# Optimization experiments

Measured on AMD Instinct MI355X. Metric: run time of the kernel, lower is better.

## Reference

```python
import jax, jax.numpy as jnp
import numpy as np

B, S, D, H = 4, 1024, 1024, 16
DK = D // H
NEG = -1e9


def setup_inputs() -> dict:
    key = jax.random.key(0)
    ks = jax.random.split(key, 8)
    inp = {
        "query": jax.random.normal(ks[0], (B, S, D), dtype=jnp.float32),
        "key": jax.random.normal(ks[1], (B, S, D), dtype=jnp.float32),
        "value": jax.random.normal(ks[2], (B, S, D), dtype=jnp.float32),
        "mask": jax.random.randint(ks[3], (B, S, S), 0, 2, dtype=jnp.int32),
        # bias-free Linear weights, torch layout [out, in]; y = x @ W.T
        "Wq": jax.random.normal(ks[4], (D, D), dtype=jnp.float32) / np.sqrt(D),
        "Wk": jax.random.normal(ks[5], (D, D), dtype=jnp.float32) / np.sqrt(D),
        "Wv": jax.random.normal(ks[6], (D, D), dtype=jnp.float32) / np.sqrt(D),
        "Wo": jax.random.normal(ks[7], (D, D), dtype=jnp.float32) / np.sqrt(D),
    }
    return inp


def _split_heads(x):
    # [B, S, D] -> [B, H, S, DK]
    return x.reshape(B, -1, H, DK).transpose(0, 2, 1, 3)


def reference(query, key, value, mask, Wq, Wk, Wv, Wo):
    q = _split_heads(query @ Wq.T)
    k = _split_heads(key @ Wk.T)
    v = _split_heads(value @ Wv.T)
    scores = jnp.einsum("bhqd,bhkd->bhqk", q, k) / jnp.sqrt(jnp.float32(DK))
    scores = jnp.where(mask[:, None, :, :] == 0, NEG, scores)
    p_attn = jax.nn.softmax(scores, axis=-1)
    x = jnp.einsum("bhqk,bhkd->bhqd", p_attn, v)
    x = x.transpose(0, 2, 1, 3).reshape(B, -1, D)
    # dropout p=0.0 (eval-equivalent): identity
    return x @ Wo.T
```

## Files before the change

kernel.cpp:

```cpp
#include <hip/hip_runtime.h>

#define BB 4
#define SS 1024
#define DD 1024
#define HH 16
#define DKK 64
#define MM (BB*SS)

typedef __bf16 bf16;
typedef __bf16 bf16x8 __attribute__((ext_vector_type(8)));
typedef float f32x4 __attribute__((ext_vector_type(4)));
typedef float f32x16 __attribute__((ext_vector_type(16)));

__device__ __forceinline__ f32x4 mfma16(bf16x8 a, bf16x8 b, f32x4 c) {
  return __builtin_amdgcn_mfma_f32_16x16x32_bf16(a, b, c, 0, 0, 0);
}
__device__ __forceinline__ f32x16 mfma32(bf16x8 a, bf16x8 b, f32x16 c) {
  return __builtin_amdgcn_mfma_f32_32x32x16_bf16(a, b, c, 0, 0, 0);
}
__device__ __forceinline__ float fexp2(float x) {
  return __builtin_amdgcn_exp2f(x);
}
__device__ __forceinline__ void gld_lds16(const bf16* g, bf16* l) {
  __builtin_amdgcn_global_load_lds(
      (const __attribute__((address_space(1))) void*)g,
      (__attribute__((address_space(3))) void*)l, 16, 0, 0);
}

__global__ __launch_bounds__(256)
void k_prep(const float* __restrict__ s0, const float* __restrict__ s1,
            const float* __restrict__ s2, const float* __restrict__ s3,
            const float* __restrict__ s4, const float* __restrict__ s5,
            const float* __restrict__ s6,
            bf16* __restrict__ d0, bf16* __restrict__ d1, bf16* __restrict__ d2,
            bf16* __restrict__ d3, bf16* __restrict__ d4, bf16* __restrict__ d5,
            bf16* __restrict__ d6,
            const int* __restrict__ mask, unsigned* __restrict__ bits) {
  const int t = blockIdx.y;
  if (t < 7) {
    const float* s = (t == 0) ? s0 : (t == 1) ? s1 : (t == 2) ? s2
                   : (t == 3) ? s3 : (t == 4) ? s4 : (t == 5) ? s5 : s6;
    bf16* d = (t == 0) ? d0 : (t == 1) ? d1 : (t == 2) ? d2
            : (t == 3) ? d3 : (t == 4) ? d4 : (t == 5) ? d5 : d6;
    const int n = (t < 3) ? (MM * DD) : (DD * DD);
    const int i0 = (blockIdx.x * 256 + threadIdx.x) * 8;
    if (i0 >= n) return;
    const f32x4 a = *(const f32x4*)(s + i0);
    const f32x4 bvv = *(const f32x4*)(s + i0 + 4);
    bf16x8 o;
#pragma unroll
    for (int j = 0; j < 4; ++j) { o[j] = (bf16)a[j]; o[4 + j] = (bf16)bvv[j]; }
    *(bf16x8*)(d + i0) = o;
    return;
  }
  const int tid = threadIdx.x;
  const int lane = tid & 63, wv = tid >> 6;
#pragma unroll
  for (int rr = 0; rr < 2; ++rr) {
    const int row = blockIdx.x * 2 + rr;
    const int b = row >> 10, q = row & 1023;
    const int qblk = q >> 6, qt = (q >> 5) & 1, l = q & 31;
    const size_t base = ((size_t)(b * 16 + qblk) * 2 + qt) * 4;
#pragma unroll
    for (int it = 0; it < 4; ++it) {
      const int cb = it * 256 + wv * 64;
      unsigned long long bal = __ballot(mask[(size_t)row * SS + cb + lane] != 0);
      if (lane == 0) {
        const int c0 = cb >> 5;
#pragma unroll
        for (int dd = 0; dd < 2; ++dd) {
          const int c = c0 + dd;
          bits[((base + (c >> 3)) * 8 + (c & 7)) * 32 + l] =
              (unsigned)(bal >> (32 * dd));
        }
      }
    }
  }
}

__global__ __launch_bounds__(256) void k_mask_bits(const int* __restrict__ mask,
                                                   unsigned* __restrict__ bits) {
  const int row = blockIdx.x;
  const int b = row >> 10, q = row & 1023;
  const int qblk = q >> 6, qt = (q >> 5) & 1, l = q & 31;
  const size_t base = ((size_t)(b * 16 + qblk) * 2 + qt) * 4;
  const int tid = threadIdx.x;
  const int lane = tid & 63, wv = tid >> 6;
#pragma unroll
  for (int it = 0; it < 4; ++it) {
    const int cb = it * 256 + wv * 64;
    unsigned long long bal = __ballot(mask[(size_t)row * SS + cb + lane] != 0);
    if (lane == 0) {
      const int c0 = cb >> 5;
#pragma unroll
      for (int dd = 0; dd < 2; ++dd) {
        const int c = c0 + dd;
        bits[((base + (c >> 3)) * 8 + (c & 7)) * 32 + l] =
            (unsigned)(bal >> (32 * dd));
      }
    }
  }
}

__global__ __launch_bounds__(256)
void k_kfrag(const bf16* __restrict__ K, bf16* __restrict__ Kf) {
  __shared__ bf16 Kl[32 * 66];
  const int kvb = blockIdx.x, h = blockIdx.y, b = blockIdx.z;
  const int tid = threadIdx.x;
  const int r = tid >> 3, c0 = (tid & 7) * 8;
  *(bf16x8*)&Kl[r * 66 + c0] =
      *(const bf16x8*)(K + (size_t)(b * SS + kvb * 32 + r) * DD + h * 64 + c0);
  __syncthreads();
  const int lane = tid & 63, l31 = lane & 31, hi = lane >> 5;
  const int kt = tid >> 6;
  bf16x8 ok;
#pragma unroll
  for (int j = 0; j < 8; ++j) ok[j] = Kl[l31 * 66 + kt * 16 + hi * 8 + j];
  *(bf16x8*)(Kf + ((size_t)((b * HH + h) * 32 + kvb)) * 2048 + tid * 8) = ok;
}

#define QSCALE 0.1803368801111204f

template<int AF32, int CF32>
__device__ __forceinline__ void gemm_body(const void* __restrict__ Ap,
                                          const float* __restrict__ Wp,
                                          void* __restrict__ Cp,
                                          int Mtot, int N, int K, int blk,
                                          float oscale) {
  __shared__ bf16 Al[128 * 40];
  __shared__ bf16 Bl[128 * 40];
  const int tid = threadIdx.x;
  const int lane = tid & 63;
  const int l15 = lane & 15, l4 = lane >> 4;
  const int wv = tid >> 6;
  const int nbm = Mtot >> 7;
  const int bm = blk % nbm, bn = blk / nbm;
  const size_t m0 = (size_t)bm << 7, n0 = (size_t)bn << 7;
  const int wr = (wv >> 1) << 6, wc = (wv & 1) << 6;
  const int srow = tid >> 2, scol = (tid & 3) << 3;

  f32x4 acc[4][4];
#pragma unroll
  for (int i = 0; i < 4; ++i)
#pragma unroll
    for (int j = 0; j < 4; ++j) acc[i][j] = f32x4{0.f, 0.f, 0.f, 0.f};

  for (int k0 = 0; k0 < K; k0 += 32) {
#pragma unroll
    for (int c = 0; c < 2; ++c) {
      const int row = (c << 6) + srow;
      bf16x8 av;
      if (AF32) {
        const float* s = (const float*)Ap + (m0 + row) * (size_t)K + k0 + scol;
        f32x4 v0 = *(const f32x4*)s;
        f32x4 v1 = *(const f32x4*)(s + 4);
#pragma unroll
        for (int j = 0; j < 4; ++j) { av[j] = (bf16)v0[j]; av[4 + j] = (bf16)v1[j]; }
      } else {
        av = *(const bf16x8*)((const bf16*)Ap + (m0 + row) * (size_t)K + k0 + scol);
      }
      *(bf16x8*)&Al[row * 40 + scol] = av;

      const float* ws_ = Wp + (n0 + row) * (size_t)K + k0 + scol;
      f32x4 w0 = *(const f32x4*)ws_;
      f32x4 w1 = *(const f32x4*)(ws_ + 4);
      bf16x8 wv8;
#pragma unroll
      for (int j = 0; j < 4; ++j) { wv8[j] = (bf16)w0[j]; wv8[4 + j] = (bf16)w1[j]; }
      *(bf16x8*)&Bl[row * 40 + scol] = wv8;
    }
    __syncthreads();

    bf16x8 af[4], bfv[4];
#pragma unroll
    for (int t = 0; t < 4; ++t) {
      af[t]  = *(const bf16x8*)&Al[(wr + t * 16 + l15) * 40 + l4 * 8];
      bfv[t] = *(const bf16x8*)&Bl[(wc + t * 16 + l15) * 40 + l4 * 8];
    }
    __builtin_amdgcn_s_setprio(1);
#pragma unroll
    for (int mt = 0; mt < 4; ++mt)
#pragma unroll
      for (int nt = 0; nt < 4; ++nt)
        acc[mt][nt] = mfma16(af[mt], bfv[nt], acc[mt][nt]);
    __builtin_amdgcn_s_setprio(0);
    __syncthreads();
  }

#pragma unroll
  for (int mt = 0; mt < 4; ++mt)
#pragma unroll
    for (int nt = 0; nt < 4; ++nt)
#pragma unroll
      for (int r = 0; r < 4; ++r) {
        const size_t row = m0 + wr + mt * 16 + l4 * 4 + r;
        const size_t col = n0 + wc + nt * 16 + l15;
        if (CF32) ((float*)Cp)[row * N + col] = acc[mt][nt][r];
        else      ((bf16*)Cp)[row * N + col] = (bf16)(acc[mt][nt][r] * oscale);
      }
}

__global__ __launch_bounds__(256)
void k_gemm_qkv(const float* __restrict__ A0, const float* __restrict__ A1,
                const float* __restrict__ A2, const float* __restrict__ W0,
                const float* __restrict__ W1, const float* __restrict__ W2,
                bf16* __restrict__ C0, bf16* __restrict__ C1, bf16* __restrict__ C2) {
  const int z = blockIdx.z;
  const float* A = (z == 0) ? A0 : (z == 1) ? A1 : A2;
  const float* W = (z == 0) ? W0 : (z == 1) ? W1 : W2;
  bf16* C = (z == 0) ? C0 : (z == 1) ? C1 : C2;
  const float sc = (z == 0) ? QSCALE : 1.0f;
  gemm_body<1, 0>(A, W, C, MM, DD, DD, blockIdx.x, sc);
}

__global__ __launch_bounds__(256)
void k_gemm_out(const bf16* __restrict__ A, const float* __restrict__ W,
                float* __restrict__ C) {
  gemm_body<0, 1>(A, W, C, MM, DD, DD, blockIdx.x, 1.0f);
}

__global__ __launch_bounds__(256)
void k_gemm_qkv_b16(const bf16* __restrict__ A0, const bf16* __restrict__ A1,
                    const bf16* __restrict__ A2, const bf16* __restrict__ W0,
                    const bf16* __restrict__ W1, const bf16* __restrict__ W2,
                    bf16* __restrict__ C0, bf16* __restrict__ Kf,
                    bf16* __restrict__ C2) {
  __shared__ bf16 Al[128 * 32];
  __shared__ bf16 Bl[128 * 32];
  const int z = blockIdx.z;
  const bf16* A = (z == 0) ? A0 : (z == 1) ? A1 : A2;
  const bf16* W = (z == 0) ? W0 : (z == 1) ? W1 : W2;
  const float oscale = (z == 0) ? QSCALE : 1.0f;

  const int tid = threadIdx.x, lane = tid & 63, w = tid >> 6;
  const int l15 = lane & 15, l4 = lane >> 4;
  const int bm = blockIdx.x & 31, bn = blockIdx.x >> 5;
  const size_t m0 = (size_t)bm << 7, n0 = (size_t)bn << 7;
  const int wr = (w >> 1) << 6, wc = (w & 1) << 6;
  const int srow = w * 32 + (lane >> 2);
  const int scol = (lane & 3) << 3;

  f32x4 acc[4][4];
#pragma unroll
  for (int i = 0; i < 4; ++i)
#pragma unroll
    for (int j = 0; j < 4; ++j) acc[i][j] = f32x4{0.f, 0.f, 0.f, 0.f};

  for (int k0 = 0; k0 < DD; k0 += 32) {
    const bf16* ga = A + (m0 + srow) * (size_t)DD + k0 + scol;
    const bf16* gb = W + (n0 + srow) * (size_t)DD + k0 + scol;
    gld_lds16(ga,            &Al[(w * 32) * 32]);
    gld_lds16(ga + 16 * DD,  &Al[(w * 32 + 16) * 32]);
    gld_lds16(gb,            &Bl[(w * 32) * 32]);
    gld_lds16(gb + 16 * DD,  &Bl[(w * 32 + 16) * 32]);
    __syncthreads();

    bf16x8 af[4], bfv[4];
#pragma unroll
    for (int t = 0; t < 4; ++t) {
      af[t]  = *(const bf16x8*)&Al[(wr + t * 16 + l15) * 32 + l4 * 8];
      bfv[t] = *(const bf16x8*)&Bl[(wc + t * 16 + l15) * 32 + l4 * 8];
    }
#pragma unroll
    for (int mt = 0; mt < 4; ++mt)
#pragma unroll
      for (int nt = 0; nt < 4; ++nt)
        acc[mt][nt] = mfma16(af[mt], bfv[nt], acc[mt][nt]);
    __syncthreads();
  }

  if (z != 1) {
    bf16* C = (z == 0) ? C0 : C2;
#pragma unroll
    for (int mt = 0; mt < 4; ++mt)
#pragma unroll
      for (int nt = 0; nt < 4; ++nt)
#pragma unroll
        for (int r = 0; r < 4; ++r) {
          const size_t row = m0 + wr + mt * 16 + l4 * 4 + r;
          const size_t col = n0 + wc + nt * 16 + l15;
          C[row * DD + col] = (bf16)(acc[mt][nt][r] * oscale);
        }
  } else {
#pragma unroll
    for (int mt = 0; mt < 4; ++mt)
#pragma unroll
      for (int nt = 0; nt < 4; ++nt)
#pragma unroll
        for (int r = 0; r < 4; ++r) {
          const int row = (int)m0 + wr + mt * 16 + l4 * 4 + r;
          const int col = (int)n0 + wc + nt * 16 + l15;
          const int b = row >> 10, kv = row & 1023;
          const int kvb = kv >> 5, l31 = kv & 31;
          const int h = col >> 6, dk = col & 63;
          const int kt = dk >> 4, hi = (dk >> 3) & 1, j = dk & 7;
          Kf[((size_t)((b * 16 + h) * 32 + kvb)) * 2048 + kt * 512 +
             (l31 + 32 * hi) * 8 + j] = (bf16)acc[mt][nt][r];
        }
  }
}

__global__ __launch_bounds__(256)
void k_gemm_out_b16(const bf16* __restrict__ A, const bf16* __restrict__ W,
                    float* __restrict__ C) {
  __shared__ bf16 Al[128 * 32];
  __shared__ bf16 Bl[128 * 32];
  const int tid = threadIdx.x, lane = tid & 63, w = tid >> 6;
  const int l15 = lane & 15, l4 = lane >> 4;
  const int bm = blockIdx.x & 31, bn = blockIdx.x >> 5;
  const size_t m0 = (size_t)bm << 7, n0 = (size_t)bn << 7;
  const int wr = (w >> 1) << 6, wc = (w & 1) << 6;
  const int srow = w * 32 + (lane >> 2);
  const int scol = (lane & 3) << 3;

  f32x4 acc[4][4];
#pragma unroll
  for (int i = 0; i < 4; ++i)
#pragma unroll
    for (int j = 0; j < 4; ++j) acc[i][j] = f32x4{0.f, 0.f, 0.f, 0.f};

  for (int k0 = 0; k0 < DD; k0 += 32) {
    const bf16* ga = A + (m0 + srow) * (size_t)DD + k0 + scol;
    const bf16* gb = W + (n0 + srow) * (size_t)DD + k0 + scol;
    gld_lds16(ga,            &Al[(w * 32) * 32]);
    gld_lds16(ga + 16 * DD,  &Al[(w * 32 + 16) * 32]);
    gld_lds16(gb,            &Bl[(w * 32) * 32]);
    gld_lds16(gb + 16 * DD,  &Bl[(w * 32 + 16) * 32]);
    __syncthreads();

    bf16x8 af[4], bfv[4];
#pragma unroll
    for (int t = 0; t < 4; ++t) {
      af[t]  = *(const bf16x8*)&Al[(wr + t * 16 + l15) * 32 + l4 * 8];
      bfv[t] = *(const bf16x8*)&Bl[(wc + t * 16 + l15) * 32 + l4 * 8];
    }
#pragma unroll
    for (int mt = 0; mt < 4; ++mt)
#pragma unroll
      for (int nt = 0; nt < 4; ++nt)
        acc[mt][nt] = mfma16(af[mt], bfv[nt], acc[mt][nt]);
    __syncthreads();
  }

#pragma unroll
  for (int mt = 0; mt < 4; ++mt)
#pragma unroll
    for (int nt = 0; nt < 4; ++nt)
#pragma unroll
      for (int r = 0; r < 4; ++r) {
        const size_t row = m0 + wr + mt * 16 + l4 * 4 + r;
        const size_t col = n0 + wc + nt * 16 + l15;
        C[row * DD + col] = acc[mt][nt][r];
      }
}

__global__ __launch_bounds__(256)
void k_attn(const bf16* __restrict__ Qw, const bf16* __restrict__ Kf,
            const bf16* __restrict__ Vw, const unsigned* __restrict__ mb,
            bf16* __restrict__ Xw) {
  __shared__ union {
    bf16 v[4][2048];
    struct { float o[64 * 33]; float l[4][64]; float inv[64]; } m;
  } sh;
  const int tid = threadIdx.x, lane = tid & 63, w = tid >> 6;
  const int l31 = lane & 31, hi = lane >> 5;
  const unsigned bid = blockIdx.x;
  const unsigned wg = (bid & 7) * 128 + (bid >> 3);
  const int bh = wg >> 4, qblk = wg & 15;
  const int h = bh & 15, b = bh >> 4;
  const int q0 = qblk * 64;

  bf16x8 qf[2][4];
#pragma unroll
  for (int qt = 0; qt < 2; ++qt) {
    const bf16* Qb = Qw + (size_t)(b * SS + q0 + qt * 32 + l31) * DD + h * 64 + hi * 8;
#pragma unroll
    for (int kt = 0; kt < 4; ++kt) qf[qt][kt] = *(const bf16x8*)(Qb + kt * 16);
  }
  const bf16* Kfb = Kf + ((size_t)((b * HH + h) * 32 + w * 8)) * 2048 + lane * 8;
  const bf16* Vg = Vw + (size_t)(b * SS) * DD + h * 64;
  const unsigned* mq0 = mb +
      ((size_t)(((b * 16 + qblk) * 2 + 0) * 4 + w) * 8) * 32 + l31;
  const unsigned* mq1 = mq0 + 1024;

  const int grow = lane >> 3;
  const int gcol = (lane & 7) * 8;
  const int kvw = w << 8;
  bf16* Vst = sh.v[w];

  f32x16 aco[2][2];
#pragma unroll
  for (int qt = 0; qt < 2; ++qt)
#pragma unroll
    for (int dt = 0; dt < 2; ++dt)
#pragma unroll
      for (int r = 0; r < 16; ++r) aco[qt][dt][r] = 0.f;
  float ssum[2] = { 0.f, 0.f };

  bf16x8 kf[4];
#pragma unroll
  for (int kt = 0; kt < 4; ++kt) kf[kt] = *(const bf16x8*)(Kfb + kt * 512);

  for (int t = 0; t < 8; ++t) {
    const int kv0 = kvw + t * 32;
#pragma unroll
    for (int i_ = 0; i_ < 4; ++i_)
      gld_lds16(Vg + (size_t)(kv0 + i_ * 8 + grow) * DD + gcol, Vst + i_ * 512);
    const unsigned mw0 = mq0[t * 32], mw1 = mq1[t * 32];

    bf16x8 va[2][2];
    union { bf16x8 v; int q[4]; } pa0[2], pa1[2];

#pragma unroll
    for (int qt = 0; qt < 2; ++qt) {
      f32x16 s;
#pragma unroll
      for (int r = 0; r < 16; ++r) s[r] = 0.f;
      __builtin_amdgcn_s_setprio(1);
#pragma unroll
      for (int kt = 0; kt < 4; ++kt) s = mfma32(kf[kt], qf[qt][kt], s);
      __builtin_amdgcn_s_setprio(0);

      if (qt == 1 && t < 7) {
        __builtin_amdgcn_sched_barrier(0);
        const bf16* tk = Kfb + (t + 1) * 2048;
#pragma unroll
        for (int kt = 0; kt < 4; ++kt) kf[kt] = *(const bf16x8*)(tk + kt * 512);
        __builtin_amdgcn_sched_barrier(0);
      }

      const unsigned mw = qt ? mw1 : mw0;
      float p[16];
#pragma unroll
      for (int r = 0; r < 16; ++r) {
        const int pos = (r & 3) + 8 * (r >> 2) + 4 * hi;
        p[r] = fexp2(((mw >> pos) & 1) ? s[r] : -1e9f);
      }
      {
        float a0 = (p[0] + p[1]) + (p[2] + p[3]);
        float a1 = (p[4] + p[5]) + (p[6] + p[7]);
        float a2 = (p[8] + p[9]) + (p[10] + p[11]);
        float a3 = (p[12] + p[13]) + (p[14] + p[15]);
        ssum[qt] += (a0 + a1) + (a2 + a3);
      }
      int dpk[8];
#pragma unroll
      for (int i = 0; i < 8; ++i) {
        union { bf16 hh[2]; int v; } u;
        u.hh[0] = (bf16)p[2 * i]; u.hh[1] = (bf16)p[2 * i + 1];
        dpk[i] = u.v;
      }
      const int sa = hi ? dpk[0] : dpk[2], sb = hi ? dpk[1] : dpk[3];
      const int sc_ = hi ? dpk[4] : dpk[6], sd = hi ? dpk[5] : dpk[7];
      const int ra = __shfl_xor(sa, 32), rb = __shfl_xor(sb, 32);
      const int rc = __shfl_xor(sc_, 32), rd = __shfl_xor(sd, 32);
      pa0[qt].q[0] = hi ? ra : dpk[0];  pa0[qt].q[1] = hi ? rb : dpk[1];
      pa0[qt].q[2] = hi ? dpk[2] : ra;  pa0[qt].q[3] = hi ? dpk[3] : rb;
      pa1[qt].q[0] = hi ? rc : dpk[4];  pa1[qt].q[1] = hi ? rd : dpk[5];
      pa1[qt].q[2] = hi ? dpk[6] : rc;  pa1[qt].q[3] = hi ? dpk[7] : rd;

      if (qt == 0) {
        asm volatile("s_waitcnt vmcnt(0)" ::: "memory");
        __builtin_amdgcn_sched_barrier(0);
#pragma unroll
        for (int dt = 0; dt < 2; ++dt)
#pragma unroll
          for (int s2 = 0; s2 < 2; ++s2) {
            bf16x8 tv;
#pragma unroll
            for (int j = 0; j < 8; ++j)
              tv[j] = Vst[(s2 * 16 + hi * 8 + j) * 64 + dt * 32 + l31];
            va[dt][s2] = tv;
          }
      }
      __builtin_amdgcn_s_setprio(1);
#pragma unroll
      for (int dt = 0; dt < 2; ++dt) {
        aco[qt][dt] = mfma32(va[dt][0], pa0[qt].v, aco[qt][dt]);
        aco[qt][dt] = mfma32(va[dt][1], pa1[qt].v, aco[qt][dt]);
      }
      __builtin_amdgcn_s_setprio(0);
    }
  }

#pragma unroll
  for (int qt = 0; qt < 2; ++qt) ssum[qt] += __shfl_xor(ssum[qt], 32);
  __syncthreads();
  if (hi == 0) {
#pragma unroll
    for (int qt = 0; qt < 2; ++qt) sh.m.l[w][qt * 32 + l31] = ssum[qt];
  }
  __syncthreads();
  if (w == 0) {
    sh.m.inv[lane] = 1.0f / (sh.m.l[0][lane] + sh.m.l[1][lane] +
                             sh.m.l[2][lane] + sh.m.l[3][lane]);
  }
  __syncthreads();
#pragma unroll
  for (int qt = 0; qt < 2; ++qt) {
    for (int rd2 = 0; rd2 < 4; ++rd2) {
      if (w == rd2) {
#pragma unroll
        for (int dt = 0; dt < 2; ++dt)
#pragma unroll
          for (int r = 0; r < 16; ++r) {
            const int d = dt * 32 + (r & 3) + 8 * (r >> 2) + 4 * hi;
            const int o = d * 33 + l31;
            if (rd2 == 0) sh.m.o[o] = aco[qt][dt][r];
            else          sh.m.o[o] += aco[qt][dt][r];
          }
      }
      __syncthreads();
    }
    {
      const int q = tid >> 3, d0 = (tid & 7) * 8;
      const float inv = sh.m.inv[qt * 32 + q];
      bf16x8 ov;
#pragma unroll
      for (int j = 0; j < 8; ++j) ov[j] = (bf16)(sh.m.o[(d0 + j) * 33 + q] * inv);
      *(bf16x8*)(Xw + (size_t)(b * SS + q0 + qt * 32 + q) * DD + h * 64 + d0) = ov;
    }
    __syncthreads();
  }
}

extern "C" void kernel_launch(void* const* d_in, const int* in_sizes, int n_in,
                              void* d_out, int out_size, void* d_ws, size_t ws_size,
                              hipStream_t stream) {
  const float* q32 = (const float*)d_in[0];
  const float* k32 = (const float*)d_in[1];
  const float* v32 = (const float*)d_in[2];
  const int* mask = (const int*)d_in[3];
  const float* Wq = (const float*)d_in[4];
  const float* Wk = (const float*)d_in[5];
  const float* Wv = (const float*)d_in[6];
  const float* Wo = (const float*)d_in[7];
  float* out = (float*)d_out;

  const size_t eAct = (size_t)MM * DD;
  const size_t eW = (size_t)DD * DD;

  bf16* Qb = (bf16*)d_ws;
  bf16* Kb = Qb + eAct;
  bf16* Vb = Kb + eAct;
  bf16* Xb = Vb + eAct;
  unsigned* mbits = (unsigned*)(Xb + eAct);
  bf16* Kfp = (bf16*)(mbits + (size_t)MM * 32);
  bf16* cvtBase = Kfp + eAct;
  bf16* Aq = cvtBase;
  bf16* Ak = Aq + eAct;
  bf16* Av = Ak + eAct;
  bf16* Wqb = Av + eAct;
  bf16* Wkb = Wqb + eW;
  bf16* Wvb = Wkb + eW;
  bf16* Wob = Wvb + eW;
  const size_t need = (size_t)((bf16*)(Wob + eW) - (bf16*)d_ws) * sizeof(bf16);

  if (ws_size >= need) {
    k_prep<<<dim3(2048, 8), 256, 0, stream>>>(q32, k32, v32, Wq, Wk, Wv, Wo,
                                              Aq, Ak, Av, Wqb, Wkb, Wvb, Wob,
                                              mask, mbits);
    k_gemm_qkv_b16<<<dim3(256, 1, 3), 256, 0, stream>>>(
        Aq, Ak, Av, Wqb, Wkb, Wvb, Qb, Kfp, Vb);
    k_attn<<<BB * HH * (SS / 64), 256, 0, stream>>>(Qb, Kfp, Vb, mbits, Xb);
    k_gemm_out_b16<<<256, 256, 0, stream>>>(Xb, Wob, out);
  } else {
    k_mask_bits<<<BB * SS, 256, 0, stream>>>(mask, mbits);
    k_gemm_qkv<<<dim3((MM / 128) * (DD / 128), 1, 3), 256, 0, stream>>>(
        q32, k32, v32, Wq, Wk, Wv, Qb, Kb, Vb);
    k_kfrag<<<dim3(32, HH, BB), 256, 0, stream>>>(Kb, Kfp);
    k_attn<<<BB * HH * (SS / 64), 256, 0, stream>>>(Qb, Kfp, Vb, mbits, Xb);
    k_gemm_out<<<(MM / 128) * (DD / 128), 256, 0, stream>>>(Xb, Wo, out);
  }
}
```

Measured before the change: 128.0 us.

## Pre-swizzle V into MFMA fragment layout and drop LDS staging in attention

The QKV GEMM epilogue now writes V directly in the per-lane MFMA fragment layout, matching how K was already stored, and the fallback path's fragment kernel handles both K and V. The attention kernel then loads V fragments with plain 16-byte global loads instead of staging V through LDS with a vmcnt wait and a per-element transposed read. K fragments are now loaded at the start of each iteration rather than prefetched one step ahead. This removes LDS traffic and a wait point, but loses the explicit K prefetch, uses more workspace, and makes the epilogue stores for V scattered.

```diff
diff --git a/kernel.cpp b/kernel.cpp
--- a/kernel.cpp
+++ b/kernel.cpp
@@ -103,20 +103,34 @@
 }
 
 __global__ __launch_bounds__(256)
-void k_kfrag(const bf16* __restrict__ K, bf16* __restrict__ Kf) {
+void k_frag(const bf16* __restrict__ K, const bf16* __restrict__ V,
+            bf16* __restrict__ Kf, bf16* __restrict__ Vf) {
   __shared__ bf16 Kl[32 * 66];
+  __shared__ bf16 Vl[32 * 66];
   const int kvb = blockIdx.x, h = blockIdx.y, b = blockIdx.z;
   const int tid = threadIdx.x;
   const int r = tid >> 3, c0 = (tid & 7) * 8;
-  *(bf16x8*)&Kl[r * 66 + c0] =
-      *(const bf16x8*)(K + (size_t)(b * SS + kvb * 32 + r) * DD + h * 64 + c0);
+  const size_t src = (size_t)(b * SS + kvb * 32 + r) * DD + h * 64 + c0;
+  *(bf16x8*)&Kl[r * 66 + c0] = *(const bf16x8*)(K + src);
+  *(bf16x8*)&Vl[r * 66 + c0] = *(const bf16x8*)(V + src);
   __syncthreads();
   const int lane = tid & 63, l31 = lane & 31, hi = lane >> 5;
-  const int kt = tid >> 6;
-  bf16x8 ok;
-#pragma unroll
-  for (int j = 0; j < 8; ++j) ok[j] = Kl[l31 * 66 + kt * 16 + hi * 8 + j];
-  *(bf16x8*)(Kf + ((size_t)((b * HH + h) * 32 + kvb)) * 2048 + tid * 8) = ok;
+  const size_t tb = ((size_t)((b * HH + h) * 32 + kvb)) * 2048 + tid * 8;
+  {
+    const int kt = tid >> 6;
+    bf16x8 ok;
+#pragma unroll
+    for (int j = 0; j < 8; ++j) ok[j] = Kl[l31 * 66 + kt * 16 + hi * 8 + j];
+    *(bf16x8*)(Kf + tb) = ok;
+  }
+  {
+    const int s2 = tid >> 7, dt = (tid >> 6) & 1;
+    bf16x8 ov;
+#pragma unroll
+    for (int j = 0; j < 8; ++j)
+      ov[j] = Vl[(s2 * 16 + hi * 8 + j) * 66 + dt * 32 + l31];
+    *(bf16x8*)(Vf + tb) = ov;
+  }
 }
 
 #define QSCALE 0.1803368801111204f
@@ -224,7 +238,7 @@
                     const bf16* __restrict__ A2, const bf16* __restrict__ W0,
                     const bf16* __restrict__ W1, const bf16* __restrict__ W2,
                     bf16* __restrict__ C0, bf16* __restrict__ Kf,
-                    bf16* __restrict__ C2) {
+                    bf16* __restrict__ Vf) {
   __shared__ bf16 Al[128 * 32];
   __shared__ bf16 Bl[128 * 32];
   const int z = blockIdx.z;
@@ -269,8 +283,7 @@
     __syncthreads();
   }
 
-  if (z != 1) {
-    bf16* C = (z == 0) ? C0 : C2;
+  if (z == 0) {
 #pragma unroll
     for (int mt = 0; mt < 4; ++mt)
 #pragma unroll
@@ -279,9 +292,9 @@
         for (int r = 0; r < 4; ++r) {
           const size_t row = m0 + wr + mt * 16 + l4 * 4 + r;
           const size_t col = n0 + wc + nt * 16 + l15;
-          C[row * DD + col] = (bf16)(acc[mt][nt][r] * oscale);
+          C0[row * DD + col] = (bf16)(acc[mt][nt][r] * oscale);
         }
-  } else {
+  } else if (z == 1) {
 #pragma unroll
     for (int mt = 0; mt < 4; ++mt)
 #pragma unroll
@@ -295,7 +308,24 @@
           const int h = col >> 6, dk = col & 63;
           const int kt = dk >> 4, hi = (dk >> 3) & 1, j = dk & 7;
           Kf[((size_t)((b * 16 + h) * 32 + kvb)) * 2048 + kt * 512 +
-             (l31 + 32 * hi) * 8 + j] = (bf16)acc[mt][nt][r];
+             (hi * 32 + l31) * 8 + j] = (bf16)acc[mt][nt][r];
+        }
+  } else {
+#pragma unroll
+    for (int mt = 0; mt < 4; ++mt)
+#pragma unroll
+      for (int nt = 0; nt < 4; ++nt)
+#pragma unroll
+        for (int r = 0; r < 4; ++r) {
+          const int row = (int)m0 + wr + mt * 16 + l4 * 4 + r;
+          const int col = (int)n0 + wc + nt * 16 + l15;
+          const int b = row >> 10, kv = row & 1023;
+          const int kvb = kv >> 5;
+          const int s2 = (kv >> 4) & 1, hi = (kv >> 3) & 1, j = kv & 7;
+          const int h = col >> 6, dk = col & 63;
+          const int dt = dk >> 5, l31 = dk & 31;
+          Vf[((size_t)((b * 16 + h) * 32 + kvb)) * 2048 + (s2 * 2 + dt) * 512 +
+             (hi * 32 + l31) * 8 + j] = (bf16)acc[mt][nt][r];
         }
   }
 }
@@ -356,12 +386,9 @@
 
 __global__ __launch_bounds__(256)
 void k_attn(const bf16* __restrict__ Qw, const bf16* __restrict__ Kf,
-            const bf16* __restrict__ Vw, const unsigned* __restrict__ mb,
+            const bf16* __restrict__ Vf, const unsigned* __restrict__ mb,
             bf16* __restrict__ Xw) {
-  __shared__ union {
-    bf16 v[4][2048];
-    struct { float o[64 * 33]; float l[4][64]; float inv[64]; } m;
-  } sh;
+  __shared__ struct { float o[64 * 33]; float l[4][64]; float inv[64]; } sh;
   const int tid = threadIdx.x, lane = tid & 63, w = tid >> 6;
   const int l31 = lane & 31, hi = lane >> 5;
   const unsigned bid = blockIdx.x;
@@ -378,16 +405,11 @@
     for (int kt = 0; kt < 4; ++kt) qf[qt][kt] = *(const bf16x8*)(Qb + kt * 16);
   }
   const bf16* Kfb = Kf + ((size_t)((b * HH + h) * 32 + w * 8)) * 2048 + lane * 8;
-  const bf16* Vg = Vw + (size_t)(b * SS) * DD + h * 64;
+  const bf16* Vfb = Vf + ((size_t)((b * HH + h) * 32 + w * 8)) * 2048 + lane * 8;
   const unsigned* mq0 = mb +
       ((size_t)(((b * 16 + qblk) * 2 + 0) * 4 + w) * 8) * 32 + l31;
   const unsigned* mq1 = mq0 + 1024;
 
-  const int grow = lane >> 3;
-  const int gcol = (lane & 7) * 8;
-  const int kvw = w << 8;
-  bf16* Vst = sh.v[w];
-
   f32x16 aco[2][2];
 #pragma unroll
   for (int qt = 0; qt < 2; ++qt)
@@ -397,15 +419,11 @@
       for (int r = 0; r < 16; ++r) aco[qt][dt][r] = 0.f;
   float ssum[2] = { 0.f, 0.f };
 
-  bf16x8 kf[4];
-#pragma unroll
-  for (int kt = 0; kt < 4; ++kt) kf[kt] = *(const bf16x8*)(Kfb + kt * 512);
-
   for (int t = 0; t < 8; ++t) {
-    const int kv0 = kvw + t * 32;
-#pragma unroll
-    for (int i_ = 0; i_ < 4; ++i_)
-      gld_lds16(Vg + (size_t)(kv0 + i_ * 8 + grow) * DD + gcol, Vst + i_ * 512);
+    const bf16* tk = Kfb + t * 2048;
+    bf16x8 kf[4];
+#pragma unroll
+    for (int kt = 0; kt < 4; ++kt) kf[kt] = *(const bf16x8*)(tk + kt * 512);
     const unsigned mw0 = mq0[t * 32], mw1 = mq1[t * 32];
 
     bf16x8 va[2][2];
@@ -421,12 +439,13 @@
       for (int kt = 0; kt < 4; ++kt) s = mfma32(kf[kt], qf[qt][kt], s);
       __builtin_amdgcn_s_setprio(0);
 
-      if (qt == 1 && t < 7) {
-        __builtin_amdgcn_sched_barrier(0);
-        const bf16* tk = Kfb + (t + 1) * 2048;
-#pragma unroll
-        for (int kt = 0; kt < 4; ++kt) kf[kt] = *(const bf16x8*)(tk + kt * 512);
-        __builtin_amdgcn_sched_barrier(0);
+      if (qt == 0) {
+        const bf16* tv = Vfb + t * 2048;
+#pragma unroll
+        for (int s2 = 0; s2 < 2; ++s2)
+#pragma unroll
+          for (int dt = 0; dt < 2; ++dt)
+            va[dt][s2] = *(const bf16x8*)(tv + (s2 * 2 + dt) * 512);
       }
 
       const unsigned mw = qt ? mw1 : mw0;
@@ -459,20 +478,6 @@
       pa1[qt].q[0] = hi ? rc : dpk[4];  pa1[qt].q[1] = hi ? rd : dpk[5];
       pa1[qt].q[2] = hi ? dpk[6] : rc;  pa1[qt].q[3] = hi ? dpk[7] : rd;
 
-      if (qt == 0) {
-        asm volatile("s_waitcnt vmcnt(0)" ::: "memory");
-        __builtin_amdgcn_sched_barrier(0);
-#pragma unroll
-        for (int dt = 0; dt < 2; ++dt)
-#pragma unroll
-          for (int s2 = 0; s2 < 2; ++s2) {
-            bf16x8 tv;
-#pragma unroll
-            for (int j = 0; j < 8; ++j)
-              tv[j] = Vst[(s2 * 16 + hi * 8 + j) * 64 + dt * 32 + l31];
-            va[dt][s2] = tv;
-          }
-      }
       __builtin_amdgcn_s_setprio(1);
 #pragma unroll
       for (int dt = 0; dt < 2; ++dt) {
@@ -488,12 +493,12 @@
   __syncthreads();
   if (hi == 0) {
 #pragma unroll
-    for (int qt = 0; qt < 2; ++qt) sh.m.l[w][qt * 32 + l31] = ssum[qt];
+    for (int qt = 0; qt < 2; ++qt) sh.l[w][qt * 32 + l31] = ssum[qt];
   }
   __syncthreads();
   if (w == 0) {
-    sh.m.inv[lane] = 1.0f / (sh.m.l[0][lane] + sh.m.l[1][lane] +
-                             sh.m.l[2][lane] + sh.m.l[3][lane]);
+    sh.inv[lane] = 1.0f / (sh.l[0][lane] + sh.l[1][lane] +
+                           sh.l[2][lane] + sh.l[3][lane]);
   }
   __syncthreads();
 #pragma unroll
@@ -506,18 +511,18 @@
           for (int r = 0; r < 16; ++r) {
             const int d = dt * 32 + (r & 3) + 8 * (r >> 2) + 4 * hi;
             const int o = d * 33 + l31;
-            if (rd2 == 0) sh.m.o[o] = aco[qt][dt][r];
-            else          sh.m.o[o] += aco[qt][dt][r];
+            if (rd2 == 0) sh.o[o] = aco[qt][dt][r];
+            else          sh.o[o] += aco[qt][dt][r];
           }
       }
       __syncthreads();
     }
     {
       const int q = tid >> 3, d0 = (tid & 7) * 8;
-      const float inv = sh.m.inv[qt * 32 + q];
+      const float inv = sh.inv[qt * 32 + q];
       bf16x8 ov;
 #pragma unroll
-      for (int j = 0; j < 8; ++j) ov[j] = (bf16)(sh.m.o[(d0 + j) * 33 + q] * inv);
+      for (int j = 0; j < 8; ++j) ov[j] = (bf16)(sh.o[(d0 + j) * 33 + q] * inv);
       *(bf16x8*)(Xw + (size_t)(b * SS + q0 + qt * 32 + q) * DD + h * 64 + d0) = ov;
     }
     __syncthreads();
@@ -546,7 +551,8 @@
   bf16* Xb = Vb + eAct;
   unsigned* mbits = (unsigned*)(Xb + eAct);
   bf16* Kfp = (bf16*)(mbits + (size_t)MM * 32);
-  bf16* cvtBase = Kfp + eAct;
+  bf16* Vfp = Kfp + eAct;
+  bf16* cvtBase = Vfp + eAct;
   bf16* Aq = cvtBase;
   bf16* Ak = Aq + eAct;
   bf16* Av = Ak + eAct;
@@ -561,15 +567,15 @@
                                               Aq, Ak, Av, Wqb, Wkb, Wvb, Wob,
                                               mask, mbits);
     k_gemm_qkv_b16<<<dim3(256, 1, 3), 256, 0, stream>>>(
-        Aq, Ak, Av, Wqb, Wkb, Wvb, Qb, Kfp, Vb);
-    k_attn<<<BB * HH * (SS / 64), 256, 0, stream>>>(Qb, Kfp, Vb, mbits, Xb);
+        Aq, Ak, Av, Wqb, Wkb, Wvb, Qb, Kfp, Vfp);
+    k_attn<<<BB * HH * (SS / 64), 256, 0, stream>>>(Qb, Kfp, Vfp, mbits, Xb);
     k_gemm_out_b16<<<256, 256, 0, stream>>>(Xb, Wob, out);
   } else {
     k_mask_bits<<<BB * SS, 256, 0, stream>>>(mask, mbits);
     k_gemm_qkv<<<dim3((MM / 128) * (DD / 128), 1, 3), 256, 0, stream>>>(
         q32, k32, v32, Wq, Wk, Wv, Qb, Kb, Vb);
-    k_kfrag<<<dim3(32, HH, BB), 256, 0, stream>>>(Kb, Kfp);
-    k_attn<<<BB * HH * (SS / 64), 256, 0, stream>>>(Qb, Kfp, Vb, mbits, Xb);
+    k_frag<<<dim3(32, HH, BB), 256, 0, stream>>>(Kb, Vb, Kfp, Vfp);
+    k_attn<<<BB * HH * (SS / 64), 256, 0, stream>>>(Qb, Kfp, Vfp, mbits, Xb);
     k_gemm_out<<<(MM / 128) * (DD / 128), 256, 0, stream>>>(Xb, Wo, out);
   }
 }
```

Result: slower. 131.2 us (+2.5%).
